# Kernel tuning notes

Hardware: AMD Instinct MI355X
Metric: run time of the kernel (lower is better)

The kernel has to match this reference:

```python
import jax, jax.numpy as jnp
import numpy as np

N = 50000      # nodes
E = 800000     # edges (before self loops)
L = 8          # backbone layers
D = 64         # gnn_in_features
F_IN = 128
F_OUT = 64
LH = 4         # learner hidden
NS = 0.2       # leaky relu negative slope
EPS = 1e-5


def setup_inputs() -> dict:
    key = jax.random.key(0)
    ks = list(jax.random.split(key, 16))
    it = iter(ks)
    rn = lambda shape, s=0.05: jax.random.normal(next(it), shape, dtype=jnp.float32) * s
    inp = {}
    inp['x'] = jax.random.normal(next(it), (N, F_IN), dtype=jnp.float32)
    inp['edge_index'] = jax.random.randint(next(it), (2, E), 0, N, dtype=jnp.int32)
    # input map: Linear(F_IN,2D) -> BN -> ReLU -> Linear(2D,D)
    inp['im_w1'] = rn((F_IN, 2 * D)); inp['im_b1'] = jnp.zeros((2 * D,), jnp.float32)
    inp['im_g1'] = jnp.ones((2 * D,), jnp.float32); inp['im_be1'] = jnp.zeros((2 * D,), jnp.float32)
    inp['im_w2'] = rn((2 * D, D)); inp['im_b2'] = jnp.zeros((D,), jnp.float32)
    # L+1 node-weight learners: Linear(D,LH) -> LeakyReLU -> Linear(LH,1) -> sigmoid
    inp['lw1'] = rn((L + 1, D, LH)); inp['lb1'] = jnp.zeros((L + 1, LH), jnp.float32)
    inp['lw2'] = rn((L + 1, LH, 1)); inp['lb2'] = jnp.zeros((L + 1, 1), jnp.float32)
    # L GCN blocks: GCNConv(D,D,bias) -> BN -> ReLU
    inp['bw'] = rn((L, D, D)); inp['bb'] = jnp.zeros((L, D), jnp.float32)
    inp['bg'] = jnp.ones((L, D), jnp.float32); inp['bbe'] = jnp.zeros((L, D), jnp.float32)
    # output map: Linear(D,2D) -> ReLU -> Linear(2D,F_OUT)  (norm='none')
    inp['om_w1'] = rn((D, 2 * D)); inp['om_b1'] = jnp.zeros((2 * D,), jnp.float32)
    inp['om_w2'] = rn((2 * D, F_OUT)); inp['om_b2'] = jnp.zeros((F_OUT,), jnp.float32)
    return inp


def _bn(h, g, b):
    mu = h.mean(0)
    var = h.var(0)
    return (h - mu) * jax.lax.rsqrt(var + EPS) * g + b


def _learner(h, w1, b1, w2, b2):
    z = jax.nn.leaky_relu(h @ w1 + b1, NS)
    return jax.nn.sigmoid(z @ w2 + b2)  # [N, 1] per-node weight


def _forward(x, edge_index,
             im_w1, im_b1, im_g1, im_be1, im_w2, im_b2,
             lw1, lb1, lw2, lb2, bw, bb, bg, bbe,
             om_w1, om_b1, om_w2, om_b2):
    loop = jnp.arange(N, dtype=edge_index.dtype)
    src = jnp.concatenate([edge_index[0], loop])  # add self loops
    dst = jnp.concatenate([edge_index[1], loop])
    deg = jax.ops.segment_sum(jnp.ones(src.shape[0], jnp.float32), dst, num_segments=N)
    dinv = jnp.where(deg > 0, jax.lax.rsqrt(jnp.maximum(deg, 1.0)), 0.0)
    enorm = (dinv[src] * dinv[dst])[:, None]  # symmetric GCN normalization

    # input map (eval mode: dropout off)
    h = jax.nn.relu(_bn(x @ im_w1 + im_b1, im_g1, im_be1)) @ im_w2 + im_b2
    h = h * _learner(h, lw1[0], lb1[0], lw2[0], lb2[0])
    fused = h
    for i in range(L):
        m = h @ bw[i]                                   # [N, D]
        agg = jax.ops.segment_sum(m[src] * enorm, dst, num_segments=N) + bb[i]
        h = jax.nn.relu(_bn(agg, bg[i], bbe[i]))
        h = h * _learner(h - fused, lw1[i + 1], lb1[i + 1], lw2[i + 1], lb2[i + 1])
        fused = fused + h
    z = jax.nn.relu(fused @ om_w1 + om_b1)
    return z @ om_w2 + om_b2


def reference(x, edge_index, im_w1, im_b1, im_g1, im_be1, im_w2, im_b2,
              lw1, lb1, lw2, lb2, bw, bb, bg, bbe,
              om_w1, om_b1, om_w2, om_b2):
    return _forward(x, edge_index, im_w1, im_b1, im_g1, im_be1, im_w2, im_b2,
                    lw1, lb1, lw2, lb2, bw, bb, bg, bbe,
                    om_w1, om_b1, om_w2, om_b2)
```

## Files before the change

kernel.cpp:

```cpp
#include <hip/hip_runtime.h>
#include <math.h>

#define Nn 50000
#define Ee 800000
#define ETe 850000
#define Dd 64
#define FIN 128
#define LL 8
#define NB 49
#define DEGB 3321
#define GEMB 782

typedef _Float16 f16;
typedef f16 f16x8 __attribute__((ext_vector_type(8)));
typedef float f32x4 __attribute__((ext_vector_type(4)));

__device__ __forceinline__ float hw_to_f(unsigned h) {
  unsigned short b = (unsigned short)(h >> 16);
  f16 w;
  __builtin_memcpy(&w, &b, 2);
  return (float)w;
}


__global__ __launch_bounds__(256) void k_prep(const float* __restrict__ W1,
    const float* __restrict__ W2, const float* __restrict__ ow1, const float* __restrict__ ow2,
    const float* __restrict__ bwA,
    f16* __restrict__ w1p, f16* __restrict__ w2p, f16* __restrict__ ow1p,
    f16* __restrict__ ow2p, f16* __restrict__ bwp) {
  int id = blockIdx.x * 256 + threadIdx.x;
  f16x8 v;
  if (id < 2176) {
    int n = id / 17, c = id % 17;
    #pragma unroll
    for (int j = 0; j < 8; ++j) v[j] = (c == 16) ? (f16)0.f : (f16)W1[(c * 8 + j) * FIN + n];
    *(f16x8*)&w1p[n * 136 + c * 8] = v;
  } else if (id < 3264) {
    int t2 = id - 2176; int n = t2 / 17, c = t2 % 17;
    #pragma unroll
    for (int j = 0; j < 8; ++j) v[j] = (c == 16) ? (f16)0.f : (f16)W2[(c * 8 + j) * Dd + n];
    *(f16x8*)&w2p[n * 136 + c * 8] = v;
  } else if (id < 4416) {
    int t2 = id - 3264; int n = t2 / 9, c = t2 % 9;
    #pragma unroll
    for (int j = 0; j < 8; ++j) v[j] = (c == 8) ? (f16)0.f : (f16)ow1[(c * 8 + j) * FIN + n];
    *(f16x8*)&ow1p[n * 72 + c * 8] = v;
  } else if (id < 5504) {
    int t2 = id - 4416; int n = t2 / 17, c = t2 % 17;
    #pragma unroll
    for (int j = 0; j < 8; ++j) v[j] = (c == 16) ? (f16)0.f : (f16)ow2[(c * 8 + j) * Dd + n];
    *(f16x8*)&ow2p[n * 136 + c * 8] = v;
  } else if (id < 10112) {
    int t2 = id - 5504; int L = t2 / 576, r = t2 % 576, n = r / 9, c = r % 9;
    #pragma unroll
    for (int j = 0; j < 8; ++j)
      v[j] = (c == 8) ? (f16)0.f : (f16)bwA[L * 4096 + (c * 8 + j) * Dd + n];
    *(f16x8*)&bwp[(size_t)L * 4608 + n * 72 + c * 8] = v;
  }
}


__global__ __launch_bounds__(256) void k_build1(const int* __restrict__ ei, int* __restrict__ deg,
    const float* __restrict__ x, const f16* __restrict__ w1p, const float* __restrict__ b1,
    f16* __restrict__ t, float* __restrict__ statS, float* __restrict__ statQ) {
  __shared__ __attribute__((aligned(16))) f16 wt[128 * 136];
  __shared__ float red[256];
  int tid = threadIdx.x;
  if (blockIdx.x < DEGB) {
    int e = blockIdx.x * 256 + tid;
    if (e < ETe) {
      int dst = (e < Ee) ? ei[Ee + e] : (e - Ee);
      atomicAdd(&deg[dst], 1);
    }
    return;
  }
  int lane = tid & 63, wid = tid >> 6;
  int row0 = (blockIdx.x - DEGB) * 64;
  red[tid] = 0.f;
  for (int i = tid; i < 2176; i += 256)
    *(f16x8*)&wt[(size_t)i * 8] = *(const f16x8*)&w1p[(size_t)i * 8];
  __syncthreads();
  int rl = lane & 15, kb = lane >> 4;
  int arow = row0 + wid * 16 + rl;
  bool rv = arow < Nn;
  f16x8 afr[4];
  #pragma unroll
  for (int ks = 0; ks < 4; ++ks) {
    float4 p0 = make_float4(0.f, 0.f, 0.f, 0.f), p1 = p0;
    if (rv) {
      p0 = *(const float4*)&x[(size_t)arow * FIN + ks * 32 + kb * 8];
      p1 = *(const float4*)&x[(size_t)arow * FIN + ks * 32 + kb * 8 + 4];
    }
    f16x8 a;
    a[0] = (f16)p0.x; a[1] = (f16)p0.y; a[2] = (f16)p0.z; a[3] = (f16)p0.w;
    a[4] = (f16)p1.x; a[5] = (f16)p1.y; a[6] = (f16)p1.z; a[7] = (f16)p1.w;
    afr[ks] = a;
  }
  f32x4 acc[8];
  #pragma unroll
  for (int i = 0; i < 8; ++i) acc[i] = (f32x4)0.f;
  #pragma unroll
  for (int ks = 0; ks < 4; ++ks) {
    #pragma unroll
    for (int ct = 0; ct < 8; ++ct) {
      f16x8 b = *(const f16x8*)&wt[(ct * 16 + rl) * 136 + ks * 32 + kb * 8];
      acc[ct] = __builtin_amdgcn_mfma_f32_16x16x32_f16(afr[ks], b, acc[ct], 0, 0, 0);
    }
  }
  #pragma unroll
  for (int ct = 0; ct < 8; ++ct) {
    int col = ct * 16 + rl;
    float bv = b1[col];
    float ps = 0.f, pq = 0.f;
    #pragma unroll
    for (int r = 0; r < 4; ++r) {
      int row = row0 + wid * 16 + kb * 4 + r;
      float v = acc[ct][r] + bv;
      if (row < Nn) {
        t[(size_t)row * FIN + col] = (f16)v;
        ps += v; pq += v * v;
      }
    }
    ps += __shfl_xor(ps, 16, 64); ps += __shfl_xor(ps, 32, 64);
    pq += __shfl_xor(pq, 16, 64); pq += __shfl_xor(pq, 32, 64);
    if (kb == 0) { atomicAdd(&red[col], ps); atomicAdd(&red[128 + col], pq); }
  }
  __syncthreads();
  if (tid < 128) {
    atomicAdd(&statS[tid], red[tid]);
    atomicAdd(&statQ[tid], red[128 + tid]);
  }
}


__global__ __launch_bounds__(1024) void k_scana(const int* __restrict__ deg,
    int* __restrict__ rowptr, int* __restrict__ bsum, float* __restrict__ dinv) {
  __shared__ int wsum[16];
  int tid = threadIdx.x, lane = tid & 63, wid = tid >> 6;
  int i = blockIdx.x * 1024 + tid;
  int v = (i < Nn) ? deg[i] : 0;
  int s = v;
  #pragma unroll
  for (int off = 1; off < 64; off <<= 1) {
    int t = __shfl_up(s, off, 64);
    if (lane >= off) s += t;
  }
  if (lane == 63) wsum[wid] = s;
  __syncthreads();
  if (wid == 0) {
    int ws = (lane < 16) ? wsum[lane] : 0;
    #pragma unroll
    for (int off = 1; off < 16; off <<= 1) {
      int t = __shfl_up(ws, off, 64);
      if (lane >= off) ws += t;
    }
    if (lane < 16) wsum[lane] = ws;
  }
  __syncthreads();
  int wexcl = (wid == 0) ? 0 : wsum[wid - 1];
  s += wexcl;
  if (i < Nn) {
    rowptr[i + 1] = s;
    dinv[i] = rsqrtf((float)v);
  }
  if (tid == 1023) bsum[blockIdx.x] = s;
}

__global__ __launch_bounds__(64) void k_scanb(const int* __restrict__ bsum, int* __restrict__ boff,
                                              int* __restrict__ rowptr) {
  int lane = threadIdx.x;
  int v = (lane < NB) ? bsum[lane] : 0;
  int s = v;
  #pragma unroll
  for (int off = 1; off < 64; off <<= 1) {
    int u = __shfl_up(s, off, 64);
    if (lane >= off) s += u;
  }
  if (lane < NB) boff[lane] = s - v;
  if (lane == 0) rowptr[0] = 0;
}

__global__ __launch_bounds__(1024) void k_scanc(int* __restrict__ rowptr, const int* __restrict__ boff) {
  int i = blockIdx.x * 1024 + threadIdx.x;
  if (i < Nn) rowptr[i + 1] += boff[blockIdx.x];
}


__global__ __launch_bounds__(256) void k_build2(const int* __restrict__ ei,
    const int* __restrict__ rowptr, int* __restrict__ fill, const float* __restrict__ dinv,
    unsigned* __restrict__ cew,
    const f16* __restrict__ t, const f16* __restrict__ w2p, const float* __restrict__ b2,
    const float* __restrict__ statS, const float* __restrict__ statQ,
    const float* __restrict__ g1, const float* __restrict__ be1,
    const float* __restrict__ lw1p, const float* __restrict__ lb1p,
    const float* __restrict__ lw2p, const float* __restrict__ lb2p,
    f16* __restrict__ fused16, f16* __restrict__ h16) {
  __shared__ __attribute__((aligned(16))) f16 w2t[64 * 136];
  __shared__ __attribute__((aligned(16))) f16 dT[64 * 72];
  __shared__ __attribute__((aligned(16))) f16 wt1[16 * 72];
  __shared__ float scs[FIN], shs[FIN], sg[64];
  int tid = threadIdx.x;
  if (blockIdx.x < DEGB) {
    int e = blockIdx.x * 256 + tid;
    if (e < ETe) {
      int src, dst;
      if (e < Ee) { src = ei[e]; dst = ei[Ee + e]; }
      else { src = e - Ee; dst = src; }
      int pos = rowptr[dst] + atomicAdd(&fill[dst], 1);
      float w = dinv[src] * dinv[dst];
      f16 wh = (f16)w;
      unsigned short wb;
      __builtin_memcpy(&wb, &wh, 2);
      cew[pos] = ((unsigned)wb << 16) | (unsigned)src;
    }
    return;
  }
  int lane = tid & 63, wid = tid >> 6;
  int row0 = (blockIdx.x - DEGB) * 64;
  for (int i = tid; i < 1088; i += 256)
    *(f16x8*)&w2t[(size_t)i * 8] = *(const f16x8*)&w2p[(size_t)i * 8];
  for (int i = tid; i < 16 * 64; i += 256) {
    int n = i & 15, k = i >> 4;
    wt1[n * 72 + k] = (n < 4) ? (f16)lw1p[k * 4 + n] : (f16)0.f;
  }
  if (tid < FIN) {
    float mu = statS[tid] * (1.f / Nn);
    float var = statQ[tid] * (1.f / Nn) - mu * mu;
    float rs = rsqrtf(var + 1e-5f);
    float scv = g1[tid] * rs;
    scs[tid] = scv; shs[tid] = be1[tid] - mu * scv;
  }
  __syncthreads();
  int rl = lane & 15, kb = lane >> 4;
  int arow = row0 + wid * 16 + rl;
  bool rv = arow < Nn;
  f16x8 afr[4];
  #pragma unroll
  for (int ks = 0; ks < 4; ++ks) {
    f16x8 tv;
    #pragma unroll
    for (int j = 0; j < 8; ++j) tv[j] = (f16)0.f;
    if (rv) tv = *(const f16x8*)(t + (size_t)arow * FIN + ks * 32 + kb * 8);
    f16x8 a;
    #pragma unroll
    for (int j = 0; j < 8; ++j) {
      int c = ks * 32 + kb * 8 + j;
      float v = fmaxf(fmaf((float)tv[j], scs[c], shs[c]), 0.f);
      a[j] = (f16)v;
    }
    afr[ks] = a;
  }
  f32x4 acc[4];
  #pragma unroll
  for (int i = 0; i < 4; ++i) acc[i] = (f32x4)0.f;
  #pragma unroll
  for (int ks = 0; ks < 4; ++ks) {
    #pragma unroll
    for (int ct = 0; ct < 4; ++ct) {
      f16x8 b = *(const f16x8*)&w2t[(ct * 16 + rl) * 136 + ks * 32 + kb * 8];
      acc[ct] = __builtin_amdgcn_mfma_f32_16x16x32_f16(afr[ks], b, acc[ct], 0, 0, 0);
    }
  }
  float b2v[4];
  #pragma unroll
  for (int ct = 0; ct < 4; ++ct) b2v[ct] = b2[ct * 16 + rl];
  #pragma unroll
  for (int ct = 0; ct < 4; ++ct)
    #pragma unroll
    for (int r = 0; r < 4; ++r)
      dT[(wid * 16 + kb * 4 + r) * 72 + ct * 16 + rl] = (f16)(acc[ct][r] + b2v[ct]);
  f32x4 zacc = (f32x4)0.f;
  #pragma unroll
  for (int ks = 0; ks < 2; ++ks) {
    f16x8 af = *(const f16x8*)&dT[(wid * 16 + rl) * 72 + ks * 32 + kb * 8];
    f16x8 bf = *(const f16x8*)&wt1[rl * 72 + ks * 32 + kb * 8];
    zacc = __builtin_amdgcn_mfma_f32_16x16x32_f16(af, bf, zacc, 0, 0, 0);
  }
  float lb1v = (rl < 4) ? lb1p[rl] : 0.f;
  float lw2v = (rl < 4) ? lw2p[rl] : 0.f;
  float lb2v = lb2p[0];
  #pragma unroll
  for (int r = 0; r < 4; ++r) {
    float z = zacc[r] + lb1v;
    z = (z > 0.f) ? z : 0.2f * z;
    float p = z * lw2v;
    p += __shfl_xor(p, 1, 64);
    p += __shfl_xor(p, 2, 64);
    float sgm = 1.f / (1.f + expf(-(p + lb2v)));
    if (rl == 0) sg[wid * 16 + kb * 4 + r] = sgm;
  }
  #pragma unroll
  for (int r = 0; r < 4; ++r) {
    int rw = row0 + wid * 16 + kb * 4 + r;
    if (rw < Nn) {
      float sgm = sg[wid * 16 + kb * 4 + r];
      #pragma unroll
      for (int ct = 0; ct < 4; ++ct) {
        float hn = (acc[ct][r] + b2v[ct]) * sgm;
        fused16[(size_t)rw * Dd + ct * 16 + rl] = (f16)hn;
        h16[(size_t)rw * Dd + ct * 16 + rl] = (f16)hn;
      }
    }
  }
}


__global__ __launch_bounds__(512) void k_agg(const f16* __restrict__ h16,
    const int* __restrict__ rowptr, const unsigned* __restrict__ cew,
    const float* __restrict__ bb, const f16* __restrict__ W16,
    f16* __restrict__ agg, float* __restrict__ statS, float* __restrict__ statQ) {
  __shared__ __attribute__((aligned(16))) f16 sumt[64 * 72];
  __shared__ __attribute__((aligned(16))) f16 wt[64 * 72];
  __shared__ float red[128];
  int tid = threadIdx.x, lane = tid & 63, wid = tid >> 6;
  int row0 = blockIdx.x * 64;
  {
    int n = tid & 63, kb8 = tid >> 6;
    *(f16x8*)&wt[n * 72 + kb8 * 8] = *(const f16x8*)&W16[n * 72 + kb8 * 8];
  }
  if (tid < 128) red[tid] = 0.f;

  int g = lane >> 3, cl = lane & 7;
  int lrow = wid * 8 + g;
  int row = row0 + lrow;
  float acc8[8];
  #pragma unroll
  for (int c = 0; c < 8; ++c) acc8[c] = 0.f;
  if (row < Nn) {
    int s0 = rowptr[row], s1 = rowptr[row + 1];
    const unsigned* ep = cew + s0;
    int n = s1 - s0;
    unsigned eh[8];
    #pragma unroll
    for (int k = 0; k < 8; ++k) eh[k] = ep[k];
    for (int j = 0; j < n; j += 8) {
      unsigned fh[8];
      #pragma unroll
      for (int k = 0; k < 8; ++k) fh[k] = ep[j + 8 + k];
      unsigned hh[8];
      #pragma unroll
      for (int k = 0; k < 8; ++k) hh[k] = (j + k < n) ? eh[k] : 0u;
      f16x8 vv[8];
      #pragma unroll
      for (int k = 0; k < 8; ++k)
        vv[k] = *(const f16x8*)(h16 + (size_t)(hh[k] & 0xffffu) * Dd + cl * 8);
      #pragma unroll
      for (int k = 0; k < 8; ++k) {
        float wk = hw_to_f(hh[k]);
        #pragma unroll
        for (int c = 0; c < 8; ++c) acc8[c] = fmaf(wk, (float)vv[k][c], acc8[c]);
      }
      #pragma unroll
      for (int k = 0; k < 8; ++k) eh[k] = fh[k];
    }
  }
  f16x8 hv;
  #pragma unroll
  for (int c = 0; c < 8; ++c) hv[c] = (f16)acc8[c];
  *(f16x8*)&sumt[lrow * 72 + cl * 8] = hv;
  __syncthreads();

  int rl = lane & 15, kb = lane >> 4;
  int strip = wid & 3, ch = wid >> 2;
  f32x4 acc0 = (f32x4)0.f, acc1v = (f32x4)0.f;
  #pragma unroll
  for (int ks = 0; ks < 2; ++ks) {
    f16x8 af = *(const f16x8*)&sumt[(strip * 16 + rl) * 72 + ks * 32 + kb * 8];
    f16x8 b0 = *(const f16x8*)&wt[((ch * 2) * 16 + rl) * 72 + ks * 32 + kb * 8];
    f16x8 b1 = *(const f16x8*)&wt[((ch * 2 + 1) * 16 + rl) * 72 + ks * 32 + kb * 8];
    acc0 = __builtin_amdgcn_mfma_f32_16x16x32_f16(af, b0, acc0, 0, 0, 0);
    acc1v = __builtin_amdgcn_mfma_f32_16x16x32_f16(af, b1, acc1v, 0, 0, 0);
  }
  #pragma unroll
  for (int t2 = 0; t2 < 2; ++t2) {
    f32x4 ac = t2 ? acc1v : acc0;
    int col = (ch * 2 + t2) * 16 + rl;
    float bv = bb[col];
    float s = 0.f, q = 0.f;
    #pragma unroll
    for (int r = 0; r < 4; ++r) {
      int rw = row0 + strip * 16 + kb * 4 + r;
      float o = ac[r] + bv;
      if (rw < Nn) {
        agg[(size_t)rw * Dd + col] = (f16)o;
        s += o; q += o * o;
      }
    }
    s += __shfl_xor(s, 16, 64); s += __shfl_xor(s, 32, 64);
    q += __shfl_xor(q, 16, 64); q += __shfl_xor(q, 32, 64);
    if (kb == 0) { atomicAdd(&red[col], s); atomicAdd(&red[64 + col], q); }
  }
  __syncthreads();
  if (tid < 64) {
    atomicAdd(&statS[tid], red[tid]);
    atomicAdd(&statQ[tid], red[64 + tid]);
  }
}


__global__ __launch_bounds__(256) void k_post(const f16* __restrict__ agg,
    const float* __restrict__ statS, const float* __restrict__ statQ,
    const float* __restrict__ gamma, const float* __restrict__ beta,
    const float* __restrict__ lw1p, const float* __restrict__ lb1p,
    const float* __restrict__ lw2p, const float* __restrict__ lb2p,
    f16* __restrict__ fused16, f16* __restrict__ h16, int mode) {
  __shared__ __attribute__((aligned(16))) f16 dT[64 * 72];
  __shared__ __attribute__((aligned(16))) f16 wt1[16 * 72];
  __shared__ float scs[Dd], shs[Dd], sg[64];
  int tid = threadIdx.x, lane = tid & 63, wid = tid >> 6;
  int row0 = blockIdx.x * 64;
  if (tid < Dd) {
    float mu = statS[tid] * (1.f / Nn);
    float var = statQ[tid] * (1.f / Nn) - mu * mu;
    float rs = rsqrtf(var + 1e-5f);
    float scv = gamma[tid] * rs;
    scs[tid] = scv; shs[tid] = beta[tid] - mu * scv;
  }
  for (int i = tid; i < 16 * 64; i += 256) {
    int n = i & 15, k = i >> 4;
    wt1[n * 72 + k] = (n < 4) ? (f16)lw1p[k * 4 + n] : (f16)0.f;
  }
  __syncthreads();
  int rw8 = lane >> 3, c8 = (lane & 7) * 8;
  float scv[8], shv[8];
  #pragma unroll
  for (int j = 0; j < 8; ++j) { scv[j] = scs[c8 + j]; shv[j] = shs[c8 + j]; }
  float hbv[2][8], fvv[2][8];
  #pragma unroll
  for (int p = 0; p < 2; ++p) {
    int lr = wid * 16 + p * 8 + rw8;
    int row = row0 + lr;
    f16x8 a8, f8;
    #pragma unroll
    for (int j = 0; j < 8; ++j) { a8[j] = (f16)0.f; f8[j] = (f16)0.f; }
    if (row < Nn) {
      a8 = *(const f16x8*)(agg + (size_t)row * Dd + c8);
      f8 = *(const f16x8*)(fused16 + (size_t)row * Dd + c8);
    }
    f16x8 d8;
    #pragma unroll
    for (int j = 0; j < 8; ++j) {
      float h = fmaxf(fmaf((float)a8[j], scv[j], shv[j]), 0.f);
      float f = (float)f8[j];
      hbv[p][j] = h; fvv[p][j] = f;
      d8[j] = (f16)(h - f);
    }
    *(f16x8*)&dT[lr * 72 + c8] = d8;
  }
  int rl = lane & 15, kb = lane >> 4;
  f32x4 zacc = (f32x4)0.f;
  #pragma unroll
  for (int ks = 0; ks < 2; ++ks) {
    f16x8 af = *(const f16x8*)&dT[(wid * 16 + rl) * 72 + ks * 32 + kb * 8];
    f16x8 bf = *(const f16x8*)&wt1[rl * 72 + ks * 32 + kb * 8];
    zacc = __builtin_amdgcn_mfma_f32_16x16x32_f16(af, bf, zacc, 0, 0, 0);
  }
  float lb1v = (rl < 4) ? lb1p[rl] : 0.f;
  float lw2v = (rl < 4) ? lw2p[rl] : 0.f;
  float lb2v = lb2p[0];
  #pragma unroll
  for (int r = 0; r < 4; ++r) {
    float z = zacc[r] + lb1v;
    z = (z > 0.f) ? z : 0.2f * z;
    float p = z * lw2v;
    p += __shfl_xor(p, 1, 64);
    p += __shfl_xor(p, 2, 64);
    float sgm = 1.f / (1.f + expf(-(p + lb2v)));
    if (rl == 0) sg[wid * 16 + kb * 4 + r] = sgm;
  }
  #pragma unroll
  for (int p = 0; p < 2; ++p) {
    int lr = wid * 16 + p * 8 + rw8;
    int row = row0 + lr;
    if (row < Nn) {
      float sgm = sg[lr];
      f16x8 ho, fo;
      #pragma unroll
      for (int j = 0; j < 8; ++j) {
        float hn = hbv[p][j] * sgm;
        float fn = fvv[p][j] + hn;
        ho[j] = (f16)hn; fo[j] = (f16)fn;
      }
      *(f16x8*)(fused16 + (size_t)row * Dd + c8) = fo;
      if (mode) *(f16x8*)(h16 + (size_t)row * Dd + c8) = ho;
    }
  }
}


__global__ __launch_bounds__(256) void k_outmap(const f16* __restrict__ fused16,
    const f16* __restrict__ ow1p, const float* __restrict__ b1,
    const f16* __restrict__ ow2p, const float* __restrict__ b2, float* __restrict__ out) {
  __shared__ __attribute__((aligned(16))) f16 fs[64 * 72];
  __shared__ __attribute__((aligned(16))) f16 w1t[128 * 72];
  __shared__ __attribute__((aligned(16))) f16 w2t[64 * 136];
  __shared__ __attribute__((aligned(16))) f16 zs[64 * 136];
  int tid = threadIdx.x, lane = tid & 63, wid = tid >> 6;
  int row0 = blockIdx.x * 64;
  for (int i = tid; i < 512; i += 256) {
    int r = i >> 3, c8 = (i & 7) * 8;
    f16x8 v;
    #pragma unroll
    for (int j = 0; j < 8; ++j) v[j] = (f16)0.f;
    if (row0 + r < Nn) v = *(const f16x8*)(fused16 + (size_t)(row0 + r) * Dd + c8);
    *(f16x8*)&fs[r * 72 + c8] = v;
  }
  for (int i = tid; i < 1152; i += 256)
    *(f16x8*)&w1t[(size_t)i * 8] = *(const f16x8*)&ow1p[(size_t)i * 8];
  for (int i = tid; i < 1088; i += 256)
    *(f16x8*)&w2t[(size_t)i * 8] = *(const f16x8*)&ow2p[(size_t)i * 8];
  __syncthreads();
  int rl = lane & 15, kb = lane >> 4;
  f32x4 acc1[8];
  #pragma unroll
  for (int i = 0; i < 8; ++i) acc1[i] = (f32x4)0.f;
  #pragma unroll
  for (int ks = 0; ks < 2; ++ks) {
    f16x8 a = *(const f16x8*)&fs[(wid * 16 + rl) * 72 + ks * 32 + kb * 8];
    #pragma unroll
    for (int ct = 0; ct < 8; ++ct) {
      f16x8 b = *(const f16x8*)&w1t[(ct * 16 + rl) * 72 + ks * 32 + kb * 8];
      acc1[ct] = __builtin_amdgcn_mfma_f32_16x16x32_f16(a, b, acc1[ct], 0, 0, 0);
    }
  }
  #pragma unroll
  for (int ct = 0; ct < 8; ++ct) {
    float bv = b1[ct * 16 + rl];
    #pragma unroll
    for (int r = 0; r < 4; ++r) {
      float z = fmaxf(acc1[ct][r] + bv, 0.f);
      zs[(wid * 16 + kb * 4 + r) * 136 + ct * 16 + rl] = (f16)z;
    }
  }
  __syncthreads();
  f32x4 acc2[4];
  #pragma unroll
  for (int i = 0; i < 4; ++i) acc2[i] = (f32x4)0.f;
  #pragma unroll
  for (int ks = 0; ks < 4; ++ks) {
    f16x8 a = *(const f16x8*)&zs[(wid * 16 + rl) * 136 + ks * 32 + kb * 8];
    #pragma unroll
    for (int ct = 0; ct < 4; ++ct) {
      f16x8 b = *(const f16x8*)&w2t[(ct * 16 + rl) * 136 + ks * 32 + kb * 8];
      acc2[ct] = __builtin_amdgcn_mfma_f32_16x16x32_f16(a, b, acc2[ct], 0, 0, 0);
    }
  }
  #pragma unroll
  for (int ct = 0; ct < 4; ++ct) {
    float bv = b2[ct * 16 + rl];
    #pragma unroll
    for (int r = 0; r < 4; ++r) {
      int row = row0 + wid * 16 + kb * 4 + r;
      if (row < Nn) out[(size_t)row * Dd + ct * 16 + rl] = acc2[ct][r] + bv;
    }
  }
}


extern "C" void kernel_launch(void* const* d_in, const int* in_sizes, int n_in,
                              void* d_out, int out_size, void* d_ws, size_t ws_size,
                              hipStream_t stream) {
  const float* x      = (const float*)d_in[0];
  const int*   ei     = (const int*)d_in[1];
  const float* im_w1  = (const float*)d_in[2];
  const float* im_b1  = (const float*)d_in[3];
  const float* im_g1  = (const float*)d_in[4];
  const float* im_be1 = (const float*)d_in[5];
  const float* im_w2  = (const float*)d_in[6];
  const float* im_b2  = (const float*)d_in[7];
  const float* lw1    = (const float*)d_in[8];
  const float* lb1    = (const float*)d_in[9];
  const float* lw2    = (const float*)d_in[10];
  const float* lb2    = (const float*)d_in[11];
  const float* bw     = (const float*)d_in[12];
  const float* bb     = (const float*)d_in[13];
  const float* bg     = (const float*)d_in[14];
  const float* bbe    = (const float*)d_in[15];
  const float* om_w1  = (const float*)d_in[16];
  const float* om_b1  = (const float*)d_in[17];
  const float* om_w2  = (const float*)d_in[18];
  const float* om_b2  = (const float*)d_in[19];
  float* out = (float*)d_out;

  char* w = (char*)d_ws;
  size_t off = 0;
  auto alloc = [&](size_t bytes) -> void* {
    void* p = w + off;
    off = (off + bytes + 255) & ~(size_t)255;
    return p;
  };
  int*   deg      = (int*)alloc((size_t)Nn * 4);
  int*   fill     = (int*)alloc((size_t)Nn * 4);
  float* statS    = (float*)alloc((size_t)9 * 128 * 4);
  float* statQ    = (float*)alloc((size_t)9 * 128 * 4);
  size_t zero_bytes = off;
  int*   rowptr   = (int*)alloc((size_t)(Nn + 1) * 4);
  int*   bsum     = (int*)alloc(64 * 4);
  int*   boff     = (int*)alloc(64 * 4);
  unsigned* cew   = (unsigned*)alloc((size_t)(ETe + 16) * 4);
  float* dinv     = (float*)alloc((size_t)Nn * 4);
  f16*   w1p      = (f16*)alloc((size_t)128 * 136 * 2);
  f16*   w2p      = (f16*)alloc((size_t)64 * 136 * 2);
  f16*   ow1p     = (f16*)alloc((size_t)128 * 72 * 2);
  f16*   ow2p     = (f16*)alloc((size_t)64 * 136 * 2);
  f16*   bwp      = (f16*)alloc((size_t)LL * 4608 * 2);
  f16*   t        = (f16*)alloc((size_t)Nn * FIN * 2);
  f16*   h16      = (f16*)alloc((size_t)Nn * Dd * 2);
  f16*   agg16    = (f16*)alloc((size_t)Nn * Dd * 2);
  f16*   fused16  = (f16*)alloc((size_t)Nn * Dd * 2);
  (void)deg; (void)fill;

  hipMemsetAsync(d_ws, 0, zero_bytes, stream);
  k_prep<<<40, 256, 0, stream>>>(im_w1, im_w2, om_w1, om_w2, bw, w1p, w2p, ow1p, ow2p, bwp);
  k_build1<<<DEGB + GEMB, 256, 0, stream>>>(ei, deg, x, w1p, im_b1, t, statS, statQ);
  k_scana<<<NB, 1024, 0, stream>>>(deg, rowptr, bsum, dinv);
  k_scanb<<<1, 64, 0, stream>>>(bsum, boff, rowptr);
  k_scanc<<<NB, 1024, 0, stream>>>(rowptr, boff);
  k_build2<<<DEGB + GEMB, 256, 0, stream>>>(ei, rowptr, fill, dinv, cew,
                                            t, w2p, im_b2, statS, statQ, im_g1, im_be1,
                                            lw1, lb1, lw2, lb2, fused16, h16);

  for (int i = 0; i < LL; ++i) {
    float* sS = statS + (size_t)(1 + i) * 128;
    float* sQ = statQ + (size_t)(1 + i) * 128;
    k_agg<<<782, 512, 0, stream>>>(h16, rowptr, cew, bb + i * Dd,
                                   bwp + (size_t)i * 4608, agg16, sS, sQ);
    k_post<<<782, 256, 0, stream>>>(agg16, sS, sQ, bg + i * Dd, bbe + i * Dd,
                                    lw1 + (size_t)(i + 1) * 256, lb1 + (size_t)(i + 1) * 4,
                                    lw2 + (size_t)(i + 1) * 4, lb2 + (i + 1),
                                    fused16, h16, (i + 1 < LL) ? 1 : 0);
  }

  k_outmap<<<782, 256, 0, stream>>>(fused16, ow1p, om_b1, ow2p, om_b2, out);
}
```

Baseline: 481.0 us.

## Software-pipeline neighbor gathers in aggregation and spread BN stat atomics across slots

The aggregation loop now issues the feature gathers for the next batch of 8 edges before doing the FMAs on the current batch, so gather latency overlaps with arithmetic. The edge-list prefetch moves two batches ahead, and the padding of the edge array grows to match. Batch-norm statistic atomics are spread over 8 slots chosen by block index, which cuts contention on the same addresses, and the consumers sum the 8 slots. The cost is more registers for the double-buffered gather vectors, which may lower occupancy.

```diff
diff --git a/kernel.cpp b/kernel.cpp
--- a/kernel.cpp
+++ b/kernel.cpp
@@ -21,6 +21,9 @@
   __builtin_memcpy(&w, &b, 2);
   return (float)w;
 }
+
+#define IMSTAT 1024
+#define LSTAT(L) (IMSTAT + (L) * 512)
 
 
 __global__ __launch_bounds__(256) void k_prep(const float* __restrict__ W1,
@@ -127,8 +130,9 @@
   }
   __syncthreads();
   if (tid < 128) {
-    atomicAdd(&statS[tid], red[tid]);
-    atomicAdd(&statQ[tid], red[128 + tid]);
+    int slot = (blockIdx.x & 7) * 128 + tid;
+    atomicAdd(&statS[slot], red[tid]);
+    atomicAdd(&statQ[slot], red[128 + tid]);
   }
 }
 
@@ -224,8 +228,11 @@
     wt1[n * 72 + k] = (n < 4) ? (f16)lw1p[k * 4 + n] : (f16)0.f;
   }
   if (tid < FIN) {
-    float mu = statS[tid] * (1.f / Nn);
-    float var = statQ[tid] * (1.f / Nn) - mu * mu;
+    float sv = 0.f, qv = 0.f;
+    #pragma unroll
+    for (int sl = 0; sl < 8; ++sl) { sv += statS[sl * 128 + tid]; qv += statQ[sl * 128 + tid]; }
+    float mu = sv * (1.f / Nn);
+    float var = qv * (1.f / Nn) - mu * mu;
     float rs = rsqrtf(var + 1e-5f);
     float scv = g1[tid] * rs;
     scs[tid] = scv; shs[tid] = be1[tid] - mu * scv;
@@ -330,28 +337,34 @@
     int s0 = rowptr[row], s1 = rowptr[row + 1];
     const unsigned* ep = cew + s0;
     int n = s1 - s0;
-    unsigned eh[8];
-    #pragma unroll
-    for (int k = 0; k < 8; ++k) eh[k] = ep[k];
+    unsigned hhA[8], ehB[8];
+    #pragma unroll
+    for (int k = 0; k < 8; ++k) hhA[k] = (k < n) ? ep[k] : 0u;
+    #pragma unroll
+    for (int k = 0; k < 8; ++k) ehB[k] = ep[8 + k];
+    f16x8 vvA[8];
+    #pragma unroll
+    for (int k = 0; k < 8; ++k)
+      vvA[k] = *(const f16x8*)(h16 + (size_t)(hhA[k] & 0xffffu) * Dd + cl * 8);
     for (int j = 0; j < n; j += 8) {
-      unsigned fh[8];
+      unsigned ehC[8];
       #pragma unroll
-      for (int k = 0; k < 8; ++k) fh[k] = ep[j + 8 + k];
-      unsigned hh[8];
+      for (int k = 0; k < 8; ++k) ehC[k] = ep[j + 16 + k];
+      unsigned hhB[8];
       #pragma unroll
-      for (int k = 0; k < 8; ++k) hh[k] = (j + k < n) ? eh[k] : 0u;
-      f16x8 vv[8];
+      for (int k = 0; k < 8; ++k) hhB[k] = (j + 8 + k < n) ? ehB[k] : 0u;
+      f16x8 vvB[8];
       #pragma unroll
       for (int k = 0; k < 8; ++k)
-        vv[k] = *(const f16x8*)(h16 + (size_t)(hh[k] & 0xffffu) * Dd + cl * 8);
+        vvB[k] = *(const f16x8*)(h16 + (size_t)(hhB[k] & 0xffffu) * Dd + cl * 8);
       #pragma unroll
       for (int k = 0; k < 8; ++k) {
-        float wk = hw_to_f(hh[k]);
+        float wk = hw_to_f(hhA[k]);
         #pragma unroll
-        for (int c = 0; c < 8; ++c) acc8[c] = fmaf(wk, (float)vv[k][c], acc8[c]);
+        for (int c = 0; c < 8; ++c) acc8[c] = fmaf(wk, (float)vvA[k][c], acc8[c]);
       }
       #pragma unroll
-      for (int k = 0; k < 8; ++k) eh[k] = fh[k];
+      for (int k = 0; k < 8; ++k) { hhA[k] = hhB[k]; vvA[k] = vvB[k]; ehB[k] = ehC[k]; }
     }
   }
   f16x8 hv;
@@ -392,8 +405,9 @@
   }
   __syncthreads();
   if (tid < 64) {
-    atomicAdd(&statS[tid], red[tid]);
-    atomicAdd(&statQ[tid], red[64 + tid]);
+    int slot = (blockIdx.x & 7) * 64 + tid;
+    atomicAdd(&statS[slot], red[tid]);
+    atomicAdd(&statQ[slot], red[64 + tid]);
   }
 }
 
@@ -410,8 +424,11 @@
   int tid = threadIdx.x, lane = tid & 63, wid = tid >> 6;
   int row0 = blockIdx.x * 64;
   if (tid < Dd) {
-    float mu = statS[tid] * (1.f / Nn);
-    float var = statQ[tid] * (1.f / Nn) - mu * mu;
+    float sv = 0.f, qv = 0.f;
+    #pragma unroll
+    for (int sl = 0; sl < 8; ++sl) { sv += statS[sl * 64 + tid]; qv += statQ[sl * 64 + tid]; }
+    float mu = sv * (1.f / Nn);
+    float var = qv * (1.f / Nn) - mu * mu;
     float rs = rsqrtf(var + 1e-5f);
     float scv = gamma[tid] * rs;
     scs[tid] = scv; shs[tid] = beta[tid] - mu * scv;
@@ -591,13 +608,13 @@
   };
   int*   deg      = (int*)alloc((size_t)Nn * 4);
   int*   fill     = (int*)alloc((size_t)Nn * 4);
-  float* statS    = (float*)alloc((size_t)9 * 128 * 4);
-  float* statQ    = (float*)alloc((size_t)9 * 128 * 4);
+  float* statS    = (float*)alloc((size_t)(IMSTAT + LL * 512) * 4);
+  float* statQ    = (float*)alloc((size_t)(IMSTAT + LL * 512) * 4);
   size_t zero_bytes = off;
   int*   rowptr   = (int*)alloc((size_t)(Nn + 1) * 4);
   int*   bsum     = (int*)alloc(64 * 4);
   int*   boff     = (int*)alloc(64 * 4);
-  unsigned* cew   = (unsigned*)alloc((size_t)(ETe + 16) * 4);
+  unsigned* cew   = (unsigned*)alloc((size_t)(ETe + 32) * 4);
   float* dinv     = (float*)alloc((size_t)Nn * 4);
   f16*   w1p      = (f16*)alloc((size_t)128 * 136 * 2);
   f16*   w2p      = (f16*)alloc((size_t)64 * 136 * 2);
@@ -621,8 +638,8 @@
                                             lw1, lb1, lw2, lb2, fused16, h16);
 
   for (int i = 0; i < LL; ++i) {
-    float* sS = statS + (size_t)(1 + i) * 128;
-    float* sQ = statQ + (size_t)(1 + i) * 128;
+    float* sS = statS + LSTAT(i);
+    float* sQ = statQ + LSTAT(i);
     k_agg<<<782, 512, 0, stream>>>(h16, rowptr, cew, bb + i * Dd,
                                    bwp + (size_t)i * 4608, agg16, sS, sQ);
     k_post<<<782, 256, 0, stream>>>(agg16, sS, sQ, bg + i * Dd, bbe + i * Dd,
```

New measurement: 401.0 us. 1.2x faster.
